# Optimization experiments

Hardware: AMD Instinct MI355X
Metric: run time of the kernel (lower is better)

## Reference

```python
import jax, jax.numpy as jnp
import numpy as np

D_MODEL = 1024
NUM_HEADS = 16
D_K = D_MODEL // NUM_HEADS


def setup_inputs() -> dict:
    key = jax.random.key(0)
    ks = jax.random.split(key, 11)
    B, S = 2, 2048
    scale = 1.0 / np.sqrt(D_MODEL)
    inp = {
        "query": jax.random.normal(ks[0], (B, S, D_MODEL), jnp.float32),
        "key": jax.random.normal(ks[1], (B, S, D_MODEL), jnp.float32),
        "value": jax.random.normal(ks[2], (B, S, D_MODEL), jnp.float32),
        "Wq": jax.random.normal(ks[3], (D_MODEL, D_MODEL), jnp.float32) * scale,
        "bq": jnp.zeros((D_MODEL,), jnp.float32),
        "Wk": jax.random.normal(ks[4], (D_MODEL, D_MODEL), jnp.float32) * scale,
        "bk": jnp.zeros((D_MODEL,), jnp.float32),
        "Wv": jax.random.normal(ks[5], (D_MODEL, D_MODEL), jnp.float32) * scale,
        "bv": jnp.zeros((D_MODEL,), jnp.float32),
        "Wo": jax.random.normal(ks[6], (D_MODEL, D_MODEL), jnp.float32) * scale,
        "bo": jnp.zeros((D_MODEL,), jnp.float32),
    }
    return inp


def _split_heads(x):
    B, S, _ = x.shape
    return x.reshape(B, S, NUM_HEADS, D_K).transpose(0, 2, 1, 3)  # [B,H,S,d_k]


def reference(query, key, value, Wq, bq, Wk, bk, Wv, bv, Wo, bo):
    # Linear projections (torch Linear: x @ W.T + b)
    q = _split_heads(query @ Wq.T + bq)
    k = _split_heads(key @ Wk.T + bk)
    v = _split_heads(value @ Wv.T + bv)
    scores = jnp.einsum("bhqd,bhkd->bhqk", q, k) / jnp.sqrt(jnp.float32(D_K))
    probs = jax.nn.softmax(scores, axis=-1)
    out = jnp.einsum("bhqk,bhkd->bhqd", probs, v)  # [B,H,S,d_k]
    B, H, S, _ = out.shape
    out = out.transpose(0, 2, 1, 3).reshape(B, S, D_MODEL)
    return out @ Wo.T + bo
```

## Files before the change

kernel.cpp:

```cpp
#include <hip/hip_runtime.h>

#define D_MODEL 1024
#define NHEADS  16
#define DK      64
#define SEQ     2048
#define NBATCH  2
#define MTOT    (NBATCH * SEQ)

typedef _Float16 f16;
typedef _Float16 f16x4 __attribute__((ext_vector_type(4)));
typedef _Float16 f16x8 __attribute__((ext_vector_type(8)));
typedef float    f32x4 __attribute__((ext_vector_type(4)));

#define LOG2E 1.44269504088896340736f

__global__ __launch_bounds__(256) void cvt_f32_to_f16(
    const float* __restrict__ q, const float* __restrict__ k, const float* __restrict__ v,
    const float* __restrict__ wq, const float* __restrict__ wk,
    const float* __restrict__ wv, const float* __restrict__ wo,
    f16* __restrict__ qf, f16* __restrict__ kf, f16* __restrict__ vf,
    f16* __restrict__ wqh, f16* __restrict__ wkh, f16* __restrict__ wvh, f16* __restrict__ woh)
{
    const int z = blockIdx.y;
    const float* src; f16* dst; int n4;
    if (z == 0)      { src = q;  dst = qf;  n4 = MTOT * D_MODEL / 4; }
    else if (z == 1) { src = k;  dst = kf;  n4 = MTOT * D_MODEL / 4; }
    else if (z == 2) { src = v;  dst = vf;  n4 = MTOT * D_MODEL / 4; }
    else if (z == 3) { src = wq; dst = wqh; n4 = D_MODEL * D_MODEL / 4; }
    else if (z == 4) { src = wk; dst = wkh; n4 = D_MODEL * D_MODEL / 4; }
    else if (z == 5) { src = wv; dst = wvh; n4 = D_MODEL * D_MODEL / 4; }
    else             { src = wo; dst = woh; n4 = D_MODEL * D_MODEL / 4; }
    for (int i = blockIdx.x * 256 + threadIdx.x; i < n4; i += gridDim.x * 256) {
        float4 t = ((const float4*)src)[i];
        f16x4 o = {(f16)t.x, (f16)t.y, (f16)t.z, (f16)t.w};
        ((f16x4*)dst)[i] = o;
    }
}

__device__ __forceinline__ void gemm128_core(
    const f16* __restrict__ A, const f16* __restrict__ Wm,
    int m0, int n0, int kbeg, int kend, f32x4 (&acc)[4][4])
{
    __shared__ __align__(16) f16 As[8192];
    __shared__ __align__(16) f16 Bs[8192];

    const int t    = threadIdx.x;
    const int lane = t & 63;
    const int w    = t >> 6;
    const int quad = lane >> 4, l15 = lane & 15;
    const int wr   = w >> 1,    wc  = w & 1;

    size_t offA[4], offB[4];
#pragma unroll
    for (int jj = 0; jj < 4; ++jj) {
        int s  = (w * 4 + jj) * 64 + lane;
        int ko = s >> 7, m = s & 127;
        offA[jj] = (size_t)(m0 + m) * D_MODEL + ko * 8;
        offB[jj] = (size_t)(n0 + m) * D_MODEL + ko * 8;
    }
    const int jb = __builtin_amdgcn_readfirstlane(w * 4 * 512);

#pragma unroll
    for (int i = 0; i < 4; ++i)
#pragma unroll
        for (int j = 0; j < 4; ++j) acc[i][j] = (f32x4){0.f, 0.f, 0.f, 0.f};

    auto* ldsA = (__attribute__((address_space(3))) f16*)As;
    auto* ldsB = (__attribute__((address_space(3))) f16*)Bs;

    for (int k0 = kbeg; k0 < kend; k0 += 64) {
#pragma unroll
        for (int jj = 0; jj < 4; ++jj) {
            __builtin_amdgcn_global_load_lds(
                (const __attribute__((address_space(1))) void*)(A + offA[jj] + k0),
                (__attribute__((address_space(3))) void*)(ldsA + jb + jj * 512),
                16, 0, 0);
            __builtin_amdgcn_global_load_lds(
                (const __attribute__((address_space(1))) void*)(Wm + offB[jj] + k0),
                (__attribute__((address_space(3))) void*)(ldsB + jb + jj * 512),
                16, 0, 0);
        }
        __syncthreads();

#pragma unroll
        for (int half = 0; half < 2; ++half) {
            f16x8 af[4], bf[4];
#pragma unroll
            for (int i = 0; i < 4; ++i) {
                const int ko = (half * 4 + quad) * 1024;
                af[i] = *(const f16x8*)&As[ko + (wr * 64 + i * 16 + l15) * 8];
                bf[i] = *(const f16x8*)&Bs[ko + (wc * 64 + i * 16 + l15) * 8];
            }
#pragma unroll
            for (int i = 0; i < 4; ++i)
#pragma unroll
                for (int j = 0; j < 4; ++j)
                    acc[i][j] = __builtin_amdgcn_mfma_f32_16x16x32_f16(af[i], bf[j], acc[i][j], 0, 0, 0);
        }
        __syncthreads();
    }
}

__global__ __launch_bounds__(256, 3) void qkv_gemm(
    const f16* __restrict__ Qf, const f16* __restrict__ Kf, const f16* __restrict__ Vf,
    const f16* __restrict__ Wqh, const f16* __restrict__ Wkh, const f16* __restrict__ Wvh,
    const float* __restrict__ bq, const float* __restrict__ bk, const float* __restrict__ bv,
    f16* __restrict__ Qh, f16* __restrict__ Kh, f16* __restrict__ Vt)
{
    const int z = blockIdx.z;
    const f16*   A    = z == 0 ? Qf  : z == 1 ? Kf  : Vf;
    const f16*   Wm   = z == 0 ? Wqh : z == 1 ? Wkh : Wvh;
    const float* bias = z == 0 ? bq  : z == 1 ? bk  : bv;

    const int m0 = blockIdx.y * 128, n0 = blockIdx.x * 128;
    f32x4 acc[4][4];
    gemm128_core(A, Wm, m0, n0, 0, D_MODEL, acc);

    const int t = threadIdx.x, lane = t & 63, w = t >> 6;
    const int quad = lane >> 4, l15 = lane & 15;
    const int wr = w >> 1, wc = w & 1;

    if (z < 2) {
        f16* Out = z == 0 ? Qh : Kh;
        const float sc = z == 0 ? 0.125f * LOG2E : 1.0f;
#pragma unroll
        for (int j = 0; j < 4; ++j) {
            const int col = n0 + wc * 64 + j * 16 + l15;
            const float bc = bias[col];
#pragma unroll
            for (int i = 0; i < 4; ++i)
#pragma unroll
                for (int r = 0; r < 4; ++r) {
                    const int row = m0 + wr * 64 + i * 16 + quad * 4 + r;
                    Out[(size_t)row * D_MODEL + col] = (f16)((acc[i][j][r] + bc) * sc);
                }
        }
    } else {
#pragma unroll
        for (int j = 0; j < 4; ++j) {
            const int col = n0 + wc * 64 + j * 16 + l15;
            const float bc = bias[col];
            const int h = col >> 6, d = col & 63;
#pragma unroll
            for (int i = 0; i < 4; ++i)
#pragma unroll
                for (int r = 0; r < 4; ++r) {
                    const int row = m0 + wr * 64 + i * 16 + quad * 4 + r;
                    const int bb = row >> 11, s = row & (SEQ - 1);
                    Vt[(size_t)((bb * NHEADS + h) * DK + d) * SEQ + s] = (f16)(acc[i][j][r] + bc);
                }
        }
    }
}

__global__ __launch_bounds__(256, 3) void oproj_splitk(
    const f16* __restrict__ A, const f16* __restrict__ Wm,
    float* __restrict__ P0, float* __restrict__ P1)
{
    const int z = blockIdx.z;
    const int m0 = blockIdx.y * 128, n0 = blockIdx.x * 128;
    f32x4 acc[4][4];
    gemm128_core(A, Wm, m0, n0, z * 512, z * 512 + 512, acc);

    float* Out = z == 0 ? P0 : P1;
    const int t = threadIdx.x, lane = t & 63, w = t >> 6;
    const int quad = lane >> 4, l15 = lane & 15;
    const int wr = w >> 1, wc = w & 1;
#pragma unroll
    for (int j = 0; j < 4; ++j) {
        const int col = n0 + wc * 64 + j * 16 + l15;
#pragma unroll
        for (int i = 0; i < 4; ++i)
#pragma unroll
            for (int r = 0; r < 4; ++r) {
                const int row = m0 + wr * 64 + i * 16 + quad * 4 + r;
                Out[(size_t)row * D_MODEL + col] = acc[i][j][r];
            }
    }
}

__global__ __launch_bounds__(256) void reduce_bias(
    const float* __restrict__ P0, const float* __restrict__ P1,
    const float* __restrict__ bias, float* __restrict__ Out)
{
    const int n4 = MTOT * D_MODEL / 4;
    for (int i = blockIdx.x * 256 + threadIdx.x; i < n4; i += gridDim.x * 256) {
        float4 a = ((const float4*)P0)[i];
        float4 b = ((const float4*)P1)[i];
        float4 c = ((const float4*)bias)[i & 255];
        float4 o = {a.x + b.x + c.x, a.y + b.y + c.y,
                    a.z + b.z + c.z, a.w + b.w + c.w};
        ((float4*)Out)[i] = o;
    }
}

__global__ __launch_bounds__(256, 2) void mha_mfma_v5(
    const f16* __restrict__ Qh, const f16* __restrict__ Kh,
    const f16* __restrict__ Vt, f16* __restrict__ Og)
{
    __shared__ __align__(16) f16 Ks[4096];
    __shared__ __align__(16) f16 Vc[4096];
    __shared__ __align__(16) f16 Ps[128 * 68];

    const int t    = threadIdx.x;
    const int w    = t >> 6;
    const int lane = t & 63;
    const int quad = lane >> 4, l15 = lane & 15;

    const int qt = blockIdx.x, bh = blockIdx.y;
    const int b  = bh >> 4,    h  = bh & 15;
    const int q0 = qt * 128;

    f16x8 aQ[2][2];
#pragma unroll
    for (int s = 0; s < 2; ++s)
#pragma unroll
        for (int c = 0; c < 2; ++c)
            aQ[s][c] = *(const f16x8*)&Qh[
                (size_t)(b * SEQ + q0 + w * 32 + s * 16 + l15) * D_MODEL
                + h * DK + c * 32 + quad * 8];

    const f16* gK[2]; const f16* gV[2]; int ldst[2];
#pragma unroll
    for (int jj = 0; jj < 2; ++jj) {
        const int kc = w * 2 + jj;
        gK[jj] = Kh + (size_t)(b * SEQ + lane) * D_MODEL + h * DK + kc * 8;
        gV[jj] = Vt + (size_t)(bh * DK + lane) * SEQ + kc * 8;
        ldst[jj] = __builtin_amdgcn_readfirstlane(kc * 512);
    }
    auto* ldsK = (__attribute__((address_space(3))) f16*)Ks;
    auto* ldsV = (__attribute__((address_space(3))) f16*)Vc;

    const f16x8 onesB = {(f16)1.f, (f16)1.f, (f16)1.f, (f16)1.f,
                         (f16)1.f, (f16)1.f, (f16)1.f, (f16)1.f};

    f32x4 o[2][4];
#pragma unroll
    for (int s = 0; s < 2; ++s)
#pragma unroll
        for (int j = 0; j < 4; ++j) o[s][j] = (f32x4){0.f, 0.f, 0.f, 0.f};
    f32x4 sacc[2] = {(f32x4){0.f, 0.f, 0.f, 0.f}, (f32x4){0.f, 0.f, 0.f, 0.f}};

    for (int kt = 0; kt < SEQ / 64; ++kt) {
#pragma unroll
        for (int jj = 0; jj < 2; ++jj) {
            __builtin_amdgcn_global_load_lds(
                (const __attribute__((address_space(1))) void*)(gK[jj] + (size_t)kt * 64 * D_MODEL),
                (__attribute__((address_space(3))) void*)(ldsK + ldst[jj]), 16, 0, 0);
            __builtin_amdgcn_global_load_lds(
                (const __attribute__((address_space(1))) void*)(gV[jj] + kt * 64),
                (__attribute__((address_space(3))) void*)(ldsV + ldst[jj]), 16, 0, 0);
        }
        __syncthreads();

        f16x8 bK[4][2], bV[4][2];
#pragma unroll
        for (int f = 0; f < 4; ++f)
#pragma unroll
            for (int c = 0; c < 2; ++c) {
                const int slot = ((c * 4 + quad) * 64 + f * 16 + l15) * 8;
                bK[f][c] = *(const f16x8*)&Ks[slot];
                bV[f][c] = *(const f16x8*)&Vc[slot];
            }

#pragma unroll
        for (int s = 0; s < 2; ++s) {
            f32x4 sc[4];
#pragma unroll
            for (int f = 0; f < 4; ++f) {
                f32x4 a = (f32x4){0.f, 0.f, 0.f, 0.f};
                a = __builtin_amdgcn_mfma_f32_16x16x32_f16(aQ[s][0], bK[f][0], a, 0, 0, 0);
                a = __builtin_amdgcn_mfma_f32_16x16x32_f16(aQ[s][1], bK[f][1], a, 0, 0, 0);
                sc[f] = a;
            }

#pragma unroll
            for (int f = 0; f < 4; ++f)
#pragma unroll
                for (int r = 0; r < 4; ++r)
                    sc[f][r] = __builtin_exp2f(sc[f][r]);

#pragma unroll
            for (int f = 0; f < 4; ++f)
#pragma unroll
                for (int r = 0; r < 4; ++r)
                    Ps[(w * 32 + s * 16 + quad * 4 + r) * 68 + f * 16 + l15] = (f16)sc[f][r];

            f16x8 aP[2];
#pragma unroll
            for (int c = 0; c < 2; ++c) {
                const int off = (w * 32 + s * 16 + l15) * 68 + c * 32 + quad * 8;
                f16x4 lo = *(const f16x4*)&Ps[off];
                f16x4 hi = *(const f16x4*)&Ps[off + 4];
                aP[c] = __builtin_shufflevector(lo, hi, 0, 1, 2, 3, 4, 5, 6, 7);
            }

#pragma unroll
            for (int j = 0; j < 4; ++j) {
                o[s][j] = __builtin_amdgcn_mfma_f32_16x16x32_f16(aP[0], bV[j][0], o[s][j], 0, 0, 0);
                o[s][j] = __builtin_amdgcn_mfma_f32_16x16x32_f16(aP[1], bV[j][1], o[s][j], 0, 0, 0);
            }
            sacc[s] = __builtin_amdgcn_mfma_f32_16x16x32_f16(aP[0], onesB, sacc[s], 0, 0, 0);
            sacc[s] = __builtin_amdgcn_mfma_f32_16x16x32_f16(aP[1], onesB, sacc[s], 0, 0, 0);
        }
        __syncthreads();
    }

#pragma unroll
    for (int s = 0; s < 2; ++s)
#pragma unroll
        for (int r = 0; r < 4; ++r) {
            const float inv = 1.f / sacc[s][r];
            const size_t row = (size_t)(b * SEQ + q0 + w * 32 + s * 16 + quad * 4 + r) * D_MODEL
                               + h * DK;
#pragma unroll
            for (int j = 0; j < 4; ++j)
                Og[row + j * 16 + l15] = (f16)(o[s][j][r] * inv);
        }
}

extern "C" void kernel_launch(void* const* d_in, const int* in_sizes, int n_in,
                              void* d_out, int out_size, void* d_ws, size_t ws_size,
                              hipStream_t stream)
{
    const float* query = (const float*)d_in[0];
    const float* key   = (const float*)d_in[1];
    const float* value = (const float*)d_in[2];
    const float* Wq    = (const float*)d_in[3];
    const float* bq    = (const float*)d_in[4];
    const float* Wk    = (const float*)d_in[5];
    const float* bk    = (const float*)d_in[6];
    const float* Wv    = (const float*)d_in[7];
    const float* bv    = (const float*)d_in[8];
    const float* Wo    = (const float*)d_in[9];
    const float* bo    = (const float*)d_in[10];
    float* out = (float*)d_out;

    f16* Qf  = (f16*)d_ws;
    f16* Kf  = Qf  + (size_t)MTOT * D_MODEL;
    f16* Vf  = Kf  + (size_t)MTOT * D_MODEL;
    f16* Wqh = Vf  + (size_t)MTOT * D_MODEL;
    f16* Wkh = Wqh + (size_t)D_MODEL * D_MODEL;
    f16* Wvh = Wkh + (size_t)D_MODEL * D_MODEL;
    f16* Woh = Wvh + (size_t)D_MODEL * D_MODEL;
    f16* Qh  = Woh + (size_t)D_MODEL * D_MODEL;
    f16* Kh  = Qh  + (size_t)MTOT * D_MODEL;
    f16* Vt  = Kh  + (size_t)MTOT * D_MODEL;
    f16* ATh = Vt  + (size_t)MTOT * D_MODEL;
    float* P0 = (float*)Qf;
    float* P1 = (float*)Qh;

    cvt_f32_to_f16<<<dim3(1024, 7), 256, 0, stream>>>(
        query, key, value, Wq, Wk, Wv, Wo, Qf, Kf, Vf, Wqh, Wkh, Wvh, Woh);

    qkv_gemm<<<dim3(D_MODEL / 128, MTOT / 128, 3), 256, 0, stream>>>(
        Qf, Kf, Vf, Wqh, Wkh, Wvh, bq, bk, bv, Qh, Kh, Vt);

    mha_mfma_v5<<<dim3(SEQ / 128, NBATCH * NHEADS), 256, 0, stream>>>(Qh, Kh, Vt, ATh);

    oproj_splitk<<<dim3(D_MODEL / 128, MTOT / 128, 2), 256, 0, stream>>>(ATh, Woh, P0, P1);

    reduce_bias<<<dim3(1024), 256, 0, stream>>>(P0, P1, bo, out);
}
```

Before: 279.3 us.

## Split attention over key halves with combine kernel; use 32x32 MFMA in GEMMs

The attention kernel now splits the key sequence into two halves across a new grid dimension. Each half writes unnormalized partial outputs and row sums, and a new combine kernel adds them and normalizes. This doubles the number of attention blocks (512 to 1024) so more work is in flight, at the cost of an extra pass over partial results. Separately, the shared GEMM core switches from 16x16x32 MFMA with 64-wide K tiles to 32x32x16 MFMA with 32-wide K tiles, halving LDS use per block but issuing twice as many syncs per K.

After: 267.2 us. 1.05x faster.

```diff
diff --git a/kernel.cpp b/kernel.cpp
--- a/kernel.cpp
+++ b/kernel.cpp
@@ -11,6 +11,7 @@
 typedef _Float16 f16x4 __attribute__((ext_vector_type(4)));
 typedef _Float16 f16x8 __attribute__((ext_vector_type(8)));
 typedef float    f32x4 __attribute__((ext_vector_type(4)));
+typedef float    f32x16 __attribute__((ext_vector_type(16)));
 
 #define LOG2E 1.44269504088896340736f
 
@@ -39,38 +40,40 @@
 
 __device__ __forceinline__ void gemm128_core(
     const f16* __restrict__ A, const f16* __restrict__ Wm,
-    int m0, int n0, int kbeg, int kend, f32x4 (&acc)[4][4])
-{
-    __shared__ __align__(16) f16 As[8192];
-    __shared__ __align__(16) f16 Bs[8192];
+    int m0, int n0, int kbeg, int kend, f32x16 (&acc)[2][2])
+{
+    __shared__ __align__(16) f16 As[4096];
+    __shared__ __align__(16) f16 Bs[4096];
 
     const int t    = threadIdx.x;
     const int lane = t & 63;
     const int w    = t >> 6;
-    const int quad = lane >> 4, l15 = lane & 15;
-    const int wr   = w >> 1,    wc  = w & 1;
-
-    size_t offA[4], offB[4];
-#pragma unroll
-    for (int jj = 0; jj < 4; ++jj) {
-        int s  = (w * 4 + jj) * 64 + lane;
+    const int l31  = lane & 31, kg = lane >> 5;
+    const int wr   = w >> 1,    wc = w & 1;
+
+    size_t offA[2], offB[2];
+#pragma unroll
+    for (int jj = 0; jj < 2; ++jj) {
+        int s  = (w * 2 + jj) * 64 + lane;
         int ko = s >> 7, m = s & 127;
         offA[jj] = (size_t)(m0 + m) * D_MODEL + ko * 8;
         offB[jj] = (size_t)(n0 + m) * D_MODEL + ko * 8;
     }
-    const int jb = __builtin_amdgcn_readfirstlane(w * 4 * 512);
-
-#pragma unroll
-    for (int i = 0; i < 4; ++i)
-#pragma unroll
-        for (int j = 0; j < 4; ++j) acc[i][j] = (f32x4){0.f, 0.f, 0.f, 0.f};
+    const int jb = __builtin_amdgcn_readfirstlane(w * 1024);
+
+#pragma unroll
+    for (int i = 0; i < 2; ++i)
+#pragma unroll
+        for (int j = 0; j < 2; ++j)
+#pragma unroll
+            for (int r = 0; r < 16; ++r) acc[i][j][r] = 0.f;
 
     auto* ldsA = (__attribute__((address_space(3))) f16*)As;
     auto* ldsB = (__attribute__((address_space(3))) f16*)Bs;
 
-    for (int k0 = kbeg; k0 < kend; k0 += 64) {
-#pragma unroll
-        for (int jj = 0; jj < 4; ++jj) {
+    for (int k0 = kbeg; k0 < kend; k0 += 32) {
+#pragma unroll
+        for (int jj = 0; jj < 2; ++jj) {
             __builtin_amdgcn_global_load_lds(
                 (const __attribute__((address_space(1))) void*)(A + offA[jj] + k0),
                 (__attribute__((address_space(3))) void*)(ldsA + jb + jj * 512),
@@ -83,19 +86,20 @@
         __syncthreads();
 
 #pragma unroll
-        for (int half = 0; half < 2; ++half) {
-            f16x8 af[4], bf[4];
-#pragma unroll
-            for (int i = 0; i < 4; ++i) {
-                const int ko = (half * 4 + quad) * 1024;
-                af[i] = *(const f16x8*)&As[ko + (wr * 64 + i * 16 + l15) * 8];
-                bf[i] = *(const f16x8*)&Bs[ko + (wc * 64 + i * 16 + l15) * 8];
-            }
-#pragma unroll
-            for (int i = 0; i < 4; ++i)
-#pragma unroll
-                for (int j = 0; j < 4; ++j)
-                    acc[i][j] = __builtin_amdgcn_mfma_f32_16x16x32_f16(af[i], bf[j], acc[i][j], 0, 0, 0);
+        for (int step = 0; step < 2; ++step) {
+            const int ko = kg + 2 * step;
+            f16x8 aF[2], bF[2];
+#pragma unroll
+            for (int ti = 0; ti < 2; ++ti) {
+                aF[ti] = *(const f16x8*)&As[(ko * 128 + wr * 64 + ti * 32 + l31) * 8];
+                bF[ti] = *(const f16x8*)&Bs[(ko * 128 + wc * 64 + ti * 32 + l31) * 8];
+            }
+#pragma unroll
+            for (int ti = 0; ti < 2; ++ti)
+#pragma unroll
+                for (int tj = 0; tj < 2; ++tj)
+                    acc[ti][tj] = __builtin_amdgcn_mfma_f32_32x32x16_f16(
+                        aF[ti], bF[tj], acc[ti][tj], 0, 0, 0);
         }
         __syncthreads();
     }
@@ -113,41 +117,41 @@
     const float* bias = z == 0 ? bq  : z == 1 ? bk  : bv;
 
     const int m0 = blockIdx.y * 128, n0 = blockIdx.x * 128;
-    f32x4 acc[4][4];
+    f32x16 acc[2][2];
     gemm128_core(A, Wm, m0, n0, 0, D_MODEL, acc);
 
     const int t = threadIdx.x, lane = t & 63, w = t >> 6;
-    const int quad = lane >> 4, l15 = lane & 15;
+    const int l31 = lane & 31, kg = lane >> 5;
     const int wr = w >> 1, wc = w & 1;
 
     if (z < 2) {
         f16* Out = z == 0 ? Qh : Kh;
         const float sc = z == 0 ? 0.125f * LOG2E : 1.0f;
 #pragma unroll
-        for (int j = 0; j < 4; ++j) {
-            const int col = n0 + wc * 64 + j * 16 + l15;
+        for (int tj = 0; tj < 2; ++tj) {
+            const int col = n0 + wc * 64 + tj * 32 + l31;
             const float bc = bias[col];
 #pragma unroll
-            for (int i = 0; i < 4; ++i)
-#pragma unroll
-                for (int r = 0; r < 4; ++r) {
-                    const int row = m0 + wr * 64 + i * 16 + quad * 4 + r;
-                    Out[(size_t)row * D_MODEL + col] = (f16)((acc[i][j][r] + bc) * sc);
+            for (int ti = 0; ti < 2; ++ti)
+#pragma unroll
+                for (int r = 0; r < 16; ++r) {
+                    const int row = m0 + wr * 64 + ti * 32 + (r & 3) + 8 * (r >> 2) + 4 * kg;
+                    Out[(size_t)row * D_MODEL + col] = (f16)((acc[ti][tj][r] + bc) * sc);
                 }
         }
     } else {
 #pragma unroll
-        for (int j = 0; j < 4; ++j) {
-            const int col = n0 + wc * 64 + j * 16 + l15;
+        for (int tj = 0; tj < 2; ++tj) {
+            const int col = n0 + wc * 64 + tj * 32 + l31;
             const float bc = bias[col];
             const int h = col >> 6, d = col & 63;
 #pragma unroll
-            for (int i = 0; i < 4; ++i)
-#pragma unroll
-                for (int r = 0; r < 4; ++r) {
-                    const int row = m0 + wr * 64 + i * 16 + quad * 4 + r;
+            for (int ti = 0; ti < 2; ++ti)
+#pragma unroll
+                for (int r = 0; r < 16; ++r) {
+                    const int row = m0 + wr * 64 + ti * 32 + (r & 3) + 8 * (r >> 2) + 4 * kg;
                     const int bb = row >> 11, s = row & (SEQ - 1);
-                    Vt[(size_t)((bb * NHEADS + h) * DK + d) * SEQ + s] = (f16)(acc[i][j][r] + bc);
+                    Vt[(size_t)((bb * NHEADS + h) * DK + d) * SEQ + s] = (f16)(acc[ti][tj][r] + bc);
                 }
         }
     }
@@ -159,22 +163,22 @@
 {
     const int z = blockIdx.z;
     const int m0 = blockIdx.y * 128, n0 = blockIdx.x * 128;
-    f32x4 acc[4][4];
+    f32x16 acc[2][2];
     gemm128_core(A, Wm, m0, n0, z * 512, z * 512 + 512, acc);
 
     float* Out = z == 0 ? P0 : P1;
     const int t = threadIdx.x, lane = t & 63, w = t >> 6;
-    const int quad = lane >> 4, l15 = lane & 15;
+    const int l31 = lane & 31, kg = lane >> 5;
     const int wr = w >> 1, wc = w & 1;
 #pragma unroll
-    for (int j = 0; j < 4; ++j) {
-        const int col = n0 + wc * 64 + j * 16 + l15;
-#pragma unroll
-        for (int i = 0; i < 4; ++i)
-#pragma unroll
-            for (int r = 0; r < 4; ++r) {
-                const int row = m0 + wr * 64 + i * 16 + quad * 4 + r;
-                Out[(size_t)row * D_MODEL + col] = acc[i][j][r];
+    for (int tj = 0; tj < 2; ++tj) {
+        const int col = n0 + wc * 64 + tj * 32 + l31;
+#pragma unroll
+        for (int ti = 0; ti < 2; ++ti)
+#pragma unroll
+            for (int r = 0; r < 16; ++r) {
+                const int row = m0 + wr * 64 + ti * 32 + (r & 3) + 8 * (r >> 2) + 4 * kg;
+                Out[(size_t)row * D_MODEL + col] = acc[ti][tj][r];
             }
     }
 }
@@ -194,9 +198,9 @@
     }
 }
 
-__global__ __launch_bounds__(256, 2) void mha_mfma_v5(
+__global__ __launch_bounds__(256, 4) void mha_mfma_v6(
     const f16* __restrict__ Qh, const f16* __restrict__ Kh,
-    const f16* __restrict__ Vt, f16* __restrict__ Og)
+    const f16* __restrict__ Vt, f16* __restrict__ Op, float* __restrict__ sp)
 {
     __shared__ __align__(16) f16 Ks[4096];
     __shared__ __align__(16) f16 Vc[4096];
@@ -207,7 +211,7 @@
     const int lane = t & 63;
     const int quad = lane >> 4, l15 = lane & 15;
 
-    const int qt = blockIdx.x, bh = blockIdx.y;
+    const int qt = blockIdx.x, bh = blockIdx.y, half = blockIdx.z;
     const int b  = bh >> 4,    h  = bh & 15;
     const int q0 = qt * 128;
 
@@ -241,7 +245,8 @@
         for (int j = 0; j < 4; ++j) o[s][j] = (f32x4){0.f, 0.f, 0.f, 0.f};
     f32x4 sacc[2] = {(f32x4){0.f, 0.f, 0.f, 0.f}, (f32x4){0.f, 0.f, 0.f, 0.f}};
 
-    for (int kt = 0; kt < SEQ / 64; ++kt) {
+    const int kt0 = half * (SEQ / 128);
+    for (int kt = kt0; kt < kt0 + SEQ / 128; ++kt) {
 #pragma unroll
         for (int jj = 0; jj < 2; ++jj) {
             __builtin_amdgcn_global_load_lds(
@@ -310,13 +315,36 @@
     for (int s = 0; s < 2; ++s)
 #pragma unroll
         for (int r = 0; r < 4; ++r) {
-            const float inv = 1.f / sacc[s][r];
-            const size_t row = (size_t)(b * SEQ + q0 + w * 32 + s * 16 + quad * 4 + r) * D_MODEL
-                               + h * DK;
+            const int qrow = q0 + w * 32 + s * 16 + quad * 4 + r;
+            const size_t base = ((size_t)(half * 32 + bh) * SEQ + qrow) * DK;
 #pragma unroll
             for (int j = 0; j < 4; ++j)
-                Og[row + j * 16 + l15] = (f16)(o[s][j][r] * inv);
-        }
+                Op[base + j * 16 + l15] = (f16)o[s][j][r];
+            if (l15 == 0)
+                sp[(size_t)(half * 32 + bh) * SEQ + qrow] = sacc[s][r];
+        }
+}
+
+__global__ __launch_bounds__(256) void mha_combine(
+    const f16* __restrict__ Op, const float* __restrict__ sp,
+    f16* __restrict__ ATh)
+{
+    const int gid = blockIdx.x * 256 + threadIdx.x;
+    const int d4 = gid & 15;
+    const int q  = (gid >> 4) & (SEQ - 1);
+    const int bh = gid >> 15;
+    const int b = bh >> 4, h = bh & 15;
+
+    const size_t i0 = ((size_t)bh * SEQ + q) * DK + d4 * 4;
+    const size_t i1 = ((size_t)(32 + bh) * SEQ + q) * DK + d4 * 4;
+    f16x4 a = *(const f16x4*)&Op[i0];
+    f16x4 c = *(const f16x4*)&Op[i1];
+    const float inv = 1.f / (sp[(size_t)bh * SEQ + q] + sp[(size_t)(32 + bh) * SEQ + q]);
+    f16x4 r;
+#pragma unroll
+    for (int m = 0; m < 4; ++m)
+        r[m] = (f16)(((float)a[m] + (float)c[m]) * inv);
+    *(f16x4*)&ATh[((size_t)(b * SEQ + q)) * D_MODEL + h * DK + d4 * 4] = r;
 }
 
 extern "C" void kernel_launch(void* const* d_in, const int* in_sizes, int n_in,
@@ -347,6 +375,9 @@
     f16* Kh  = Qh  + (size_t)MTOT * D_MODEL;
     f16* Vt  = Kh  + (size_t)MTOT * D_MODEL;
     f16* ATh = Vt  + (size_t)MTOT * D_MODEL;
+
+    f16*   Op = Qf;
+    float* sp = (float*)(Vf + (size_t)1024 * 1024);
     float* P0 = (float*)Qf;
     float* P1 = (float*)Qh;
 
@@ -356,7 +387,10 @@
     qkv_gemm<<<dim3(D_MODEL / 128, MTOT / 128, 3), 256, 0, stream>>>(
         Qf, Kf, Vf, Wqh, Wkh, Wvh, bq, bk, bv, Qh, Kh, Vt);
 
-    mha_mfma_v5<<<dim3(SEQ / 128, NBATCH * NHEADS), 256, 0, stream>>>(Qh, Kh, Vt, ATh);
+    mha_mfma_v6<<<dim3(SEQ / 128, NBATCH * NHEADS, 2), 256, 0, stream>>>(
+        Qh, Kh, Vt, Op, sp);
+
+    mha_combine<<<dim3(MTOT * D_MODEL / 4 / 256), 256, 0, stream>>>(Op, sp, ATh);
 
     oproj_splitk<<<dim3(D_MODEL / 128, MTOT / 128, 2), 256, 0, stream>>>(ATh, Woh, P0, P1);
 
```
